# Kernel tuning notes

Hardware: AMD Instinct MI355X
Metric: run time of the kernel (lower is better)

## Reference

```python
import jax, jax.numpy as jnp
import numpy as np

B, V, C, NQ, H, PTS, FFN = 2, 6, 128, 1200, 8, 4, 256
SHAPES = [(112, 200), (56, 100), (28, 50), (14, 25)]
LVLS = len(SHAPES)
LTOT = sum(h * w for h, w in SHAPES)
STARTS = np.cumsum([0] + [h * w for h, w in SHAPES])[:-1].tolist()


def _ln(x, g, b):
    m = jnp.mean(x, -1, keepdims=True)
    v = jnp.var(x, -1, keepdims=True)
    return (x - m) * jax.lax.rsqrt(v + 1e-5) * g + b


def _mlp(x, w1, b1, w2, b2):
    return jax.nn.relu(x @ w1 + b1) @ w2 + b2


def setup_inputs():
    ks = iter(jax.random.split(jax.random.key(0), 64))
    def rn(*shape):
        return jax.random.normal(next(ks), shape, jnp.float32) * 0.02
    inp = {}
    inp["img_query_feat"] = jax.random.normal(next(ks), (B, C, NQ), jnp.float32)
    inp["normal_img_query_pos"] = jax.random.normal(next(ks), (B, NQ, 2), jnp.float32)
    for i, (h, w) in enumerate(SHAPES):
        inp["img_feat%d" % i] = jax.random.normal(next(ks), (B, V, C, h, w), jnp.float32)
    inp["normal_img_feats_pos_stack"] = jax.random.uniform(next(ks), (1, LTOT, 2), jnp.float32)
    inp["sp_w1"] = rn(2, C); inp["sp_b1"] = rn(C); inp["sp_w2"] = rn(C, C); inp["sp_b2"] = rn(C)
    inp["cp_w1"] = rn(2, C); inp["cp_b1"] = rn(C); inp["cp_w2"] = rn(C, C); inp["cp_b2"] = rn(C)
    inp["sa_wqkv"] = rn(C, 3 * C); inp["sa_bqkv"] = rn(3 * C); inp["sa_wo"] = rn(C, C); inp["sa_bo"] = rn(C)
    inp["ln1_g"] = jnp.ones((C,), jnp.float32); inp["ln1_b"] = jnp.zeros((C,), jnp.float32)
    inp["d_val_w"] = rn(C, C); inp["d_val_b"] = rn(C)
    inp["d_off_w"] = rn(C, H * LVLS * PTS * 2); inp["d_off_b"] = rn(H * LVLS * PTS * 2)
    inp["d_attn_w"] = rn(C, H * LVLS * PTS); inp["d_attn_b"] = rn(H * LVLS * PTS)
    inp["d_out_w"] = rn(C, C); inp["d_out_b"] = rn(C)
    inp["ln2_g"] = jnp.ones((C,), jnp.float32); inp["ln2_b"] = jnp.zeros((C,), jnp.float32)
    inp["ffn_w1"] = rn(C, FFN); inp["ffn_b1"] = rn(FFN); inp["ffn_w2"] = rn(FFN, C); inp["ffn_b2"] = rn(C)
    inp["ln3_g"] = jnp.ones((C,), jnp.float32); inp["ln3_b"] = jnp.zeros((C,), jnp.float32)
    inp["ph_w1"] = rn(C, C); inp["ph_b1"] = rn(C); inp["ph_w2"] = rn(C, 6); inp["ph_b2"] = rn(6)
    inp["img_query_view"] = jax.random.randint(next(ks), (B, NQ), 0, V)
    return inp


def _forward(img_query_view, img_query_feat, normal_img_query_pos, img_feat0, img_feat1, img_feat2, img_feat3, normal_img_feats_pos_stack, sp_w1, sp_b1, sp_w2, sp_b2, cp_w1, cp_b1, cp_w2, cp_b2, sa_wqkv, sa_bqkv, sa_wo, sa_bo, ln1_g, ln1_b, d_val_w, d_val_b, d_off_w, d_off_b, d_attn_w, d_attn_b, d_out_w, d_out_b, ln2_g, ln2_b, ffn_w1, ffn_b1, ffn_w2, ffn_b2, ln3_g, ln3_b, ph_w1, ph_b1, ph_w2, ph_b2):
    # flatten multi-scale feats: [B, V, C, LTOT]
    feats = jnp.concatenate([f.reshape(B, V, C, -1) for f in (img_feat0, img_feat1, img_feat2, img_feat3)], axis=3)
    ref = jax.nn.sigmoid(normal_img_query_pos)  # [B,NQ,2], shared across levels
    qpe = _mlp(normal_img_query_pos, sp_w1, sp_b1, sp_w2, sp_b2)  # [B,NQ,C] self posembed
    kpe = _mlp(normal_img_feats_pos_stack[0], cp_w1, cp_b1, cp_w2, cp_b2)  # [LTOT,C] cross posembed
    # value projection of (key + key_pos_embed), per view
    value = jnp.einsum('bvcl,cd->bvld', feats, d_val_w) + kpe @ d_val_w + d_val_b  # [B,V,LTOT,C]
    value_flat = value.reshape(B, V * LTOT, C)
    x = img_query_feat.transpose(0, 2, 1)  # [B,NQ,C]
    # ragged per-view grouping: queries interact only within their own view
    same_view = img_query_view[:, :, None] == img_query_view[:, None, :]
    counts = jax.vmap(lambda v: jnp.bincount(v, length=V))(img_query_view)  # [B,V]
    valid = jnp.take_along_axis(counts, img_query_view, axis=1) > 1  # views with <=1 query are skipped
    Ch = C // H
    # --- self attention (masked to same view) ---
    qkv = (x + qpe) @ sa_wqkv + sa_bqkv
    q, k, v = jnp.split(qkv, 3, axis=-1)
    q = q.reshape(B, NQ, H, Ch); k = k.reshape(B, NQ, H, Ch); v = v.reshape(B, NQ, H, Ch)
    logits = jnp.einsum('bnhd,bmhd->bhnm', q, k) / float(np.sqrt(Ch))
    logits = jnp.where(same_view[:, None], logits, -1e9)
    attn = jax.nn.softmax(logits, axis=-1)
    sa_out = jnp.einsum('bhnm,bmhd->bnhd', attn, v).reshape(B, NQ, C) @ sa_wo + sa_bo
    x = _ln(x + sa_out, ln1_g, ln1_b)
    # --- multi-scale deformable cross attention, view-routed per query ---
    qc = x + qpe
    off = (qc @ d_off_w + d_off_b).reshape(B, NQ, H, LVLS, PTS, 2)
    aw = jax.nn.softmax((qc @ d_attn_w + d_attn_b).reshape(B, NQ, H, LVLS * PTS), axis=-1).reshape(B, NQ, H, LVLS, PTS)
    normalizer = jnp.array([[w, h] for h, w in SHAPES], jnp.float32)  # (w,h) per level
    loc = ref[:, :, None, None, None, :] + off / normalizer[None, None, None, :, None, :]
    base = (img_query_view * LTOT)[:, :, None, None].astype(jnp.int32)  # route query to its view
    eyeH = jnp.eye(H, dtype=x.dtype)
    out = jnp.zeros((B, NQ, H, Ch), x.dtype)
    for l, (h, w) in enumerate(SHAPES):
        lx = loc[:, :, :, l, :, 0] * w - 0.5  # grid_sample align_corners=False convention
        ly = loc[:, :, :, l, :, 1] * h - 0.5  # [B,NQ,H,PTS]
        x0 = jnp.floor(lx); y0 = jnp.floor(ly)
        fx = lx - x0; fy = ly - y0
        x0i = x0.astype(jnp.int32); y0i = y0.astype(jnp.int32)
        samp = jnp.zeros((B, NQ, H, PTS, Ch), x.dtype)
        for dy in (0, 1):
            for dx in (0, 1):
                xi = x0i + dx; yi = y0i + dy
                wgt = (fx if dx else 1.0 - fx) * (fy if dy else 1.0 - fy)
                ok = (xi >= 0) & (xi < w) & (yi >= 0) & (yi < h)  # zero padding
                idx = base + STARTS[l] + jnp.clip(yi, 0, h - 1) * w + jnp.clip(xi, 0, w - 1)
                g = jnp.take_along_axis(value_flat, idx.reshape(B, -1)[:, :, None], axis=1)
                g = g.reshape(B, NQ, H, PTS, H, Ch)
                g = jnp.einsum('bnhpqc,hq->bnhpc', g, eyeH)  # head h uses its own channel slice
                samp = samp + jnp.where(ok[..., None], wgt[..., None], 0.0) * g
        out = out + jnp.einsum('bnhp,bnhpc->bnhc', aw[:, :, :, l], samp)
    ca_out = out.reshape(B, NQ, C) @ d_out_w + d_out_b
    x = _ln(x + ca_out, ln2_g, ln2_b)
    x = _ln(x + _mlp(x, ffn_w1, ffn_b1, ffn_w2, ffn_b2), ln3_g, ln3_b)
    x = jnp.where(valid[..., None], x, 0.0)  # skipped views stay zero (scatter-back semantics)
    # --- prediction head: center_offset [B,6,NQ] ---
    res = _mlp(x, ph_w1, ph_b1, ph_w2, ph_b2).transpose(0, 2, 1)
    center_raw = res[:, :2] + normal_img_query_pos.transpose(0, 2, 1)
    new_pos = jax.lax.stop_gradient(center_raw).transpose(0, 2, 1)  # supervision2d=True update
    center = jax.nn.sigmoid(center_raw)
    offs = jax.nn.sigmoid(res[:, 2:])
    bw = offs[:, 0] + offs[:, 2]
    bh = offs[:, 1] + offs[:, 3]
    cx = (2.0 * center[:, 0] - offs[:, 0] + offs[:, 2]) * 0.5
    cy = (2.0 * center[:, 1] - offs[:, 1] + offs[:, 3]) * 0.5
    bbox = jax.lax.stop_gradient(jnp.stack([cx, cy, bw, bh], axis=1))
    return (x.transpose(0, 2, 1), new_pos, center, offs, bbox)


def reference(img_query_feat, normal_img_query_pos, img_feat0, img_feat1, img_feat2, img_feat3, normal_img_feats_pos_stack, sp_w1, sp_b1, sp_w2, sp_b2, cp_w1, cp_b1, cp_w2, cp_b2, sa_wqkv, sa_bqkv, sa_wo, sa_bo, ln1_g, ln1_b, d_val_w, d_val_b, d_off_w, d_off_b, d_attn_w, d_attn_b, d_out_w, d_out_b, ln2_g, ln2_b, ffn_w1, ffn_b1, ffn_w2, ffn_b2, ln3_g, ln3_b, ph_w1, ph_b1, ph_w2, ph_b2, img_query_view):
    return _forward(img_query_view, img_query_feat, normal_img_query_pos, img_feat0, img_feat1, img_feat2, img_feat3, normal_img_feats_pos_stack, sp_w1, sp_b1, sp_w2, sp_b2, cp_w1, cp_b1, cp_w2, cp_b2, sa_wqkv, sa_bqkv, sa_wo, sa_bo, ln1_g, ln1_b, d_val_w, d_val_b, d_off_w, d_off_b, d_attn_w, d_attn_b, d_out_w, d_out_b, ln2_g, ln2_b, ffn_w1, ffn_b1, ffn_w2, ffn_b2, ln3_g, ln3_b, ph_w1, ph_b1, ph_w2, ph_b2)
```

## Files before the change

### kernel.cpp

```cpp
#include <hip/hip_runtime.h>
#include <hip/hip_bf16.h>
#include <math.h>

#define DEV __device__ __forceinline__

#define BB 2
#define VV 6
#define CC 128
#define NQ 1200
#define HH 8
#define PTSN 4
#define FFND 256
#define LVLSN 4
#define LTOT 29750
#define NROWS (BB*NQ)

__constant__ int c_W[4] = {200,100,50,25};
__constant__ int c_H[4] = {112,56,28,14};
__constant__ int c_S[4] = {0,22400,28000,29400};

DEV float bflo(unsigned u){ union{unsigned i; float f;}x; x.i = u<<16; return x.f; }
DEV float bfhi(unsigned u){ union{unsigned i; float f;}x; x.i = u&0xffff0000u; return x.f; }
DEV unsigned short f2bf(float f){ union{float f; unsigned i;}x; x.f=f; unsigned i=x.i;
  return (unsigned short)((i + 0x7fffu + ((i>>16)&1u))>>16); }
DEV unsigned addbf2(unsigned a, unsigned b){
  float lo = bflo(a)+bflo(b); float hi = bfhi(a)+bfhi(b);
  return (unsigned)f2bf(lo) | ((unsigned)f2bf(hi)<<16);
}
DEV float sigm(float z){ return 1.f/(1.f+__expf(-z)); }

typedef __attribute__((ext_vector_type(8))) short bf16x8;
typedef __attribute__((ext_vector_type(4))) float f32x4;

__global__ void k_misc(const int* __restrict__ view, int* __restrict__ order,
                       int* __restrict__ counts,
                       const float* __restrict__ vw, unsigned short* __restrict__ wt,
                       const float* __restrict__ cw2, unsigned short* __restrict__ cw2t,
                       const float* __restrict__ iqf, float* __restrict__ x,
                       const float* __restrict__ pos,
                       const float* __restrict__ w1, const float* __restrict__ b1,
                       const float* __restrict__ w2, const float* __restrict__ b2,
                       float* __restrict__ qpe){
  int bid = blockIdx.x;
  int t = threadIdx.x;
  if(bid < BB){
    if(t < 64){
      int b = bid; int lane = t;
      int base0=0,base1=0,base2=0,base3=0,base4=0,base5=0;
      for(int c0=0;c0<NQ;c0+=64){
        int n = c0 + lane;
        int v = (n<NQ) ? view[b*NQ+n] : -1;
        unsigned long long lower = (lane==63)? 0x7fffffffffffffffull : ((1ull<<lane)-1ull);
        #define BUCKET_STEP(VVV, BASE) { \
          unsigned long long mk = __ballot(v==VVV); \
          if(v==VVV){ int r = BASE + __popcll(mk & lower); order[(b*VV+VVV)*NQ + r] = n; } \
          BASE += __popcll(mk); }
        BUCKET_STEP(0, base0) BUCKET_STEP(1, base1) BUCKET_STEP(2, base2)
        BUCKET_STEP(3, base3) BUCKET_STEP(4, base4) BUCKET_STEP(5, base5)
        #undef BUCKET_STEP
      }
      if(lane==0){
        counts[b*VV+0]=base0; counts[b*VV+1]=base1; counts[b*VV+2]=base2;
        counts[b*VV+3]=base3; counts[b*VV+4]=base4; counts[b*VV+5]=base5;
      }
    }
  } else if(bid < BB+16){
    int d0 = (bid-BB)*8;
    __shared__ float s[128][9];
    #pragma unroll
    for(int p=0;p<4;p++){ int i = t + p*256; int c = i>>3, dd = i&7;
      s[c][dd] = vw[c*128 + d0 + dd]; }
    __syncthreads();
    #pragma unroll
    for(int p=0;p<4;p++){ int i = t + p*256; int dd = i>>7, c = i&127;
      wt[(size_t)(d0+dd)*128 + c] = f2bf(s[c][dd]); }
  } else if(bid < BB+32){
    int d0 = (bid-BB-16)*8;
    __shared__ float s[128][9];
    #pragma unroll
    for(int p=0;p<4;p++){ int i = t + p*256; int c = i>>3, dd = i&7;
      s[c][dd] = cw2[c*128 + d0 + dd]; }
    __syncthreads();
    #pragma unroll
    for(int p=0;p<4;p++){ int i = t + p*256; int dd = i>>7, c = i&127;
      cw2t[(size_t)(d0+dd)*128 + c] = f2bf(s[c][dd]); }
  } else if(bid < BB+32+76){
    __shared__ float tile[128][33];
    int idx = bid - (BB+32);
    int b = idx/38; int n0 = (idx%38)*32;
    for(int i=t;i<128*32;i+=256){ int c=i>>5, nn=i&31; int n=n0+nn;
      tile[c][nn] = (n<NQ)? iqf[((size_t)b*CC + c)*NQ + n] : 0.f; }
    __syncthreads();
    for(int i=t;i<32*128;i+=256){ int nn=i>>7, c=i&127;
      int n=n0+nn; if(n<NQ) x[((size_t)b*NQ+n)*128 + c] = tile[c][nn]; }
  } else {
    __shared__ float hid[4][128];
    int row0 = (bid - (BB+32+76))*4;
    int r = t>>7, d = t&127;
    #pragma unroll
    for(int rr=r; rr<4; rr+=2){
      int row = row0 + rr;
      float p0 = pos[row*2+0], p1 = pos[row*2+1];
      hid[rr][d] = fmaxf(p0*w1[d] + p1*w1[128+d] + b1[d], 0.f);
    }
    __syncthreads();
    #pragma unroll
    for(int rr=r; rr<4; rr+=2){
      float acc = b2[d];
      #pragma unroll 4
      for(int c=0;c<128;c++) acc += hid[rr][c]*w2[c*128 + d];
      qpe[(size_t)(row0+rr)*128+d] = acc;
    }
  }
}

__global__ void __launch_bounds__(256) k_kvpe2(
    const float* __restrict__ kpos,
    const float* __restrict__ cw1, const float* __restrict__ cb1,
    const unsigned short* __restrict__ cw2t, const float* __restrict__ cb2,
    const unsigned short* __restrict__ wt, const float* __restrict__ vb,
    unsigned short* __restrict__ kvpe){
  __shared__ unsigned short h_t[64][136];
  __shared__ unsigned short k_t[64][136];
  int t = threadIdx.x;
  int r0 = blockIdx.x*64;
  int lane = t&63, wave = t>>6;
  int fr = lane&15, kg = lane>>4;

  int p = t & 63;
  int d0 = p*2;
  float w1a0 = cw1[d0],     w1a1 = cw1[d0+1];
  float w1b0 = cw1[128+d0], w1b1 = cw1[128+d0+1];
  float b10 = cb1[d0], b11 = cb1[d0+1];
  #pragma unroll 4
  for(int k=0;k<16;k++){
    int r = wave + k*4;
    int row = r0 + r;
    float p0=0.f, p1=0.f;
    if(row < LTOT){ p0 = kpos[row*2]; p1 = kpos[row*2+1]; }
    float h0 = fmaxf(p0*w1a0 + p1*w1b0 + b10, 0.f);
    float h1 = fmaxf(p0*w1a1 + p1*w1b1 + b11, 0.f);
    *reinterpret_cast<unsigned*>(&h_t[r][d0]) = (unsigned)f2bf(h0) | ((unsigned)f2bf(h1)<<16);
  }
  __syncthreads();

  f32x4 acc[4][2];
  #pragma unroll
  for(int i=0;i<4;i++)
    #pragma unroll
    for(int j=0;j<2;j++) acc[i][j] = (f32x4)0.f;
  #pragma unroll
  for(int ck=0; ck<4; ck++){
    int c0 = ck*32;
    bf16x8 bfr[2], af[4];
    #pragma unroll
    for(int j=0;j<2;j++){ int d = wave*32 + j*16 + fr;
      bfr[j] = *reinterpret_cast<const bf16x8*>(cw2t + (size_t)d*128 + c0 + kg*8); }
    #pragma unroll
    for(int i=0;i<4;i++) af[i] = *reinterpret_cast<const bf16x8*>(&h_t[i*16 + fr][c0 + kg*8]);
    #pragma unroll
    for(int i=0;i<4;i++)
      #pragma unroll
      for(int j=0;j<2;j++)
        acc[i][j] = __builtin_amdgcn_mfma_f32_16x16x32_bf16(af[i], bfr[j], acc[i][j], 0, 0, 0);
  }
  #pragma unroll
  for(int i=0;i<4;i++){
    int rbase = i*16 + kg*4;
    #pragma unroll
    for(int j=0;j<2;j++){
      int d = wave*32 + j*16 + fr;
      float bv_ = cb2[d];
      #pragma unroll
      for(int r=0;r<4;r++) k_t[rbase + r][d] = f2bf(acc[i][j][r] + bv_);
    }
  }
  __syncthreads();

  #pragma unroll
  for(int i=0;i<4;i++)
    #pragma unroll
    for(int j=0;j<2;j++) acc[i][j] = (f32x4)0.f;
  #pragma unroll
  for(int ck=0; ck<4; ck++){
    int c0 = ck*32;
    bf16x8 bfr[2], af[4];
    #pragma unroll
    for(int j=0;j<2;j++){ int d = wave*32 + j*16 + fr;
      bfr[j] = *reinterpret_cast<const bf16x8*>(wt + (size_t)d*128 + c0 + kg*8); }
    #pragma unroll
    for(int i=0;i<4;i++) af[i] = *reinterpret_cast<const bf16x8*>(&k_t[i*16 + fr][c0 + kg*8]);
    #pragma unroll
    for(int i=0;i<4;i++)
      #pragma unroll
      for(int j=0;j<2;j++)
        acc[i][j] = __builtin_amdgcn_mfma_f32_16x16x32_bf16(af[i], bfr[j], acc[i][j], 0, 0, 0);
  }
  __syncthreads();
  unsigned short (*c_l)[136] = h_t;
  #pragma unroll
  for(int i=0;i<4;i++){
    int rbase = i*16 + kg*4;
    #pragma unroll
    for(int j=0;j<2;j++){
      int d = wave*32 + j*16 + fr;
      float bv_ = vb[d];
      #pragma unroll
      for(int r=0;r<4;r++) c_l[rbase + r][d] = f2bf(acc[i][j][r] + bv_);
    }
  }
  __syncthreads();
  #pragma unroll
  for(int p4=0;p4<4;p4++){
    int i = t + p4*256;
    int row = i>>4, seg = i&15;
    int glr = r0 + row;
    if(glr < LTOT){
      uint4 cu = *reinterpret_cast<const uint4*>(&c_l[row][seg*8]);
      *reinterpret_cast<uint4*>(kvpe + (size_t)glr*CC + seg*8) = cu;
    }
  }
}

#define QKVB 300
__global__ void __launch_bounds__(256) k_value_qkv(
    const float* __restrict__ f0, const float* __restrict__ f1,
    const float* __restrict__ f2, const float* __restrict__ f3,
    const unsigned short* __restrict__ kvpe, const unsigned short* __restrict__ wt,
    unsigned short* __restrict__ value,
    const float* __restrict__ x, const float* __restrict__ qpe,
    const float* __restrict__ sa_wqkv, const float* __restrict__ sa_bqkv,
    float* __restrict__ qkv){
  __shared__ unsigned short a_t[64][136];
  __shared__ float s_q[8][128];
  int t = threadIdx.x;
  int bid = blockIdx.x;
  if(bid < QKVB){
    int r0 = bid*8;
    for(int i=t;i<1024;i+=256){ int r=i>>7, c=i&127;
      size_t row = (size_t)(r0+r);
      s_q[r][c] = x[row*128+c] + qpe[row*128+c]; }
    __syncthreads();
    for(int d=t; d<384; d+=256){
      float acc[8];
      #pragma unroll
      for(int r=0;r<8;r++) acc[r]=sa_bqkv[d];
      #pragma unroll 4
      for(int c=0;c<128;c++){ float wv = sa_wqkv[c*384+d];
        #pragma unroll
        for(int r=0;r<8;r++) acc[r] += s_q[r][c]*wv; }
      #pragma unroll
      for(int r=0;r<8;r++) qkv[(size_t)(r0+r)*384+d]=acc[r];
    }
    return;
  }
  int bxy = bid - QKVB;
  int bv = bxy % 12;
  int bx = bxy / 12;
  int lvl, tile;
  if(bx < 350){ lvl=0; tile=bx; }
  else if(bx < 438){ lvl=1; tile=bx-350; }
  else if(bx < 460){ lvl=2; tile=bx-438; }
  else { lvl=3; tile=bx-460; }
  const int HW = (lvl==0)?22400:(lvl==1)?5600:(lvl==2)?1400:350;
  const int startL = (lvl==0)?0:(lvl==1)?22400:(lvl==2)?28000:29400;
  const float* feat = (lvl==0)?f0:(lvl==1)?f1:(lvl==2)?f2:f3;
  const float* fbase = feat + (size_t)bv*128*(size_t)HW;
  int l0 = tile*64;

  int lane = t&63, wave = t>>6;
  int fr = lane&15, kg = lane>>4;

  int l_u = t & 63, oct0 = t>>6;
  int gl = l0 + l_u; bool ok = (gl < HW);
  const float* fcol = fbase + (size_t)(oct0*8)*HW + (ok ? gl : 0);

  float v32[4][8];
  #pragma unroll
  for(int q=0;q<4;q++)
    #pragma unroll
    for(int j=0;j<8;j++)
      v32[q][j] = ok ? fcol[(size_t)(q*32+j)*HW] : 0.f;

  #pragma unroll
  for(int q=0;q<4;q++){
    uint4 u;
    u.x = (unsigned)f2bf(v32[q][0]) | ((unsigned)f2bf(v32[q][1])<<16);
    u.y = (unsigned)f2bf(v32[q][2]) | ((unsigned)f2bf(v32[q][3])<<16);
    u.z = (unsigned)f2bf(v32[q][4]) | ((unsigned)f2bf(v32[q][5])<<16);
    u.w = (unsigned)f2bf(v32[q][6]) | ((unsigned)f2bf(v32[q][7])<<16);
    *reinterpret_cast<uint4*>(&a_t[l_u][oct0*8 + q*32]) = u;
  }
  __syncthreads();

  f32x4 acc[4][2];
  #pragma unroll
  for(int i=0;i<4;i++)
    #pragma unroll
    for(int j=0;j<2;j++) acc[i][j] = (f32x4)0.f;

  #pragma unroll
  for(int ck=0; ck<4; ck++){
    int c0 = ck*32;
    bf16x8 bfr[2];
    #pragma unroll
    for(int j=0;j<2;j++){
      int d = wave*32 + j*16 + fr;
      bfr[j] = *reinterpret_cast<const bf16x8*>(wt + (size_t)d*128 + c0 + kg*8);
    }
    bf16x8 af[4];
    #pragma unroll
    for(int i=0;i<4;i++) af[i] = *reinterpret_cast<const bf16x8*>(&a_t[i*16 + fr][c0 + kg*8]);
    #pragma unroll
    for(int i=0;i<4;i++)
      #pragma unroll
      for(int j=0;j<2;j++)
        acc[i][j] = __builtin_amdgcn_mfma_f32_16x16x32_bf16(af[i], bfr[j], acc[i][j], 0, 0, 0);
  }

  __syncthreads();
  unsigned short (*c_l)[136] = a_t;
  #pragma unroll
  for(int i=0;i<4;i++){
    int rbase = i*16 + kg*4;
    #pragma unroll
    for(int j=0;j<2;j++){
      int d = wave*32 + j*16 + fr;
      #pragma unroll
      for(int r=0;r<4;r++) c_l[rbase + r][d] = f2bf(acc[i][j][r]);
    }
  }
  __syncthreads();
  #pragma unroll
  for(int p=0;p<4;p++){
    int i = t + p*256;
    int row = i>>4, seg = i&15;
    int glr = l0 + row;
    if(glr < HW){
      uint4 cu = *reinterpret_cast<const uint4*>(&c_l[row][seg*8]);
      const uint4 ku = *reinterpret_cast<const uint4*>(kvpe + (size_t)(startL+glr)*CC + seg*8);
      uint4 ou;
      ou.x = addbf2(cu.x, ku.x); ou.y = addbf2(cu.y, ku.y);
      ou.z = addbf2(cu.z, ku.z); ou.w = addbf2(cu.w, ku.w);
      *reinterpret_cast<uint4*>(value + ((size_t)bv*LTOT + startL + glr)*CC + seg*8) = ou;
    }
  }
}

#define QT2 64
#define KT2 128
__global__ void __launch_bounds__(256) k_attn_v(const float* __restrict__ qkv,
        const int* __restrict__ order, const int* __restrict__ counts,
        float* __restrict__ att){
  int qt = blockIdx.x;
  int vh = blockIdx.y; int v = vh>>3, h = vh&7;
  int b = blockIdx.z;
  int C = counts[b*VV+v];
  int q0 = qt*QT2;
  if(q0 >= C) return;
  const int* ord = order + (size_t)(b*VV+v)*NQ;
  int t = threadIdx.x;
  __shared__ float q_s[QT2][17];
  __shared__ int qn_s[QT2];
  __shared__ float k_s[KT2][16];
  __shared__ float v_s[KT2][16];
  __shared__ float red[4][QT2][18];
  for(int i=t;i<QT2;i+=256){ int qi=q0+i; qn_s[i] = (qi<C)? ord[qi] : -1; }
  __syncthreads();
  for(int i=t;i<QT2*16;i+=256){ int r=i>>4,c=i&15; int n=qn_s[r];
    q_s[r][c] = (n>=0)? qkv[((size_t)b*NQ+n)*384 + h*16 + c] : 0.f; }
  int qi = t&63, sub = t>>6;
  float m = -1e30f, s = 0.f, acc[16];
  #pragma unroll
  for(int c=0;c<16;c++) acc[c]=0.f;
  for(int k0=0; k0<C; k0+=KT2){
    int kn = C-k0; if(kn>KT2) kn=KT2;
    __syncthreads();
    for(int i=t;i<KT2*16;i+=256){ int r=i>>4,c=i&15;
      float kv=0.f, vv=0.f;
      if(r<kn){ int n=ord[k0+r]; size_t base=((size_t)b*NQ+n)*384 + h*16 + c;
        kv = qkv[base+128]; vv = qkv[base+256]; }
      k_s[r][c]=kv; v_s[r][c]=vv; }
    __syncthreads();
    for(int mm=sub; mm<kn; mm+=4){
      float l=0.f;
      #pragma unroll
      for(int c=0;c<16;c++) l += q_s[qi][c]*k_s[mm][c];
      l *= 0.25f;
      float newm = fmaxf(m,l);
      float e = __expf(l - newm);
      if(newm > m){
        float rr = __expf(m - newm);
        s *= rr;
        #pragma unroll
        for(int c=0;c<16;c++) acc[c]*=rr;
        m = newm;
      }
      s += e;
      #pragma unroll
      for(int c=0;c<16;c++) acc[c] += e*v_s[mm][c];
    }
  }
  red[sub][qi][0]=m; red[sub][qi][1]=s;
  #pragma unroll
  for(int c=0;c<16;c++) red[sub][qi][2+c]=acc[c];
  __syncthreads();
  if(sub==0){
    int n = qn_s[qi];
    if(n>=0){
      float M=-1e30f;
      #pragma unroll
      for(int j=0;j<4;j++) M=fmaxf(M,red[j][qi][0]);
      float S=0.f; float o[16];
      #pragma unroll
      for(int c=0;c<16;c++) o[c]=0.f;
      #pragma unroll
      for(int j=0;j<4;j++){ float e=__expf(red[j][qi][0]-M); S += e*red[j][qi][1];
        #pragma unroll
        for(int c=0;c<16;c++) o[c] += e*red[j][qi][2+c]; }
      float inv = 1.f/S;
      #pragma unroll
      for(int c=0;c<16;c++) att[((size_t)b*NQ+n)*128 + h*16 + c] = o[c]*inv;
    }
  }
}

__global__ void __launch_bounds__(384) k_q2(
    const float* __restrict__ att, const float* __restrict__ sa_wo, const float* __restrict__ sa_bo,
    float* __restrict__ x, const float* __restrict__ ln1_g, const float* __restrict__ ln1_b,
    const float* __restrict__ qpe,
    const float* __restrict__ dow, const float* __restrict__ dob,
    const float* __restrict__ daw, const float* __restrict__ dab,
    float* __restrict__ offb, float* __restrict__ awb){
  int r0 = blockIdx.x*8; int t = threadIdx.x;
  __shared__ float s_att[8][128];
  __shared__ float s_qc[8][128];
  __shared__ float s_m[8][2][2];
  __shared__ float s_aw[8][130];
  for(int i=t;i<1024;i+=384){ int r=i>>7, c=i&127; s_att[r][c]=att[(size_t)(r0+r)*128+c]; }
  __syncthreads();
  int lane = t&63, wid = (t>>6)&1;
  float v[8];
  if(t < 128){
    int d = t;
    float acc[8];
    #pragma unroll
    for(int r=0;r<8;r++) acc[r]=sa_bo[d];
    #pragma unroll 4
    for(int c=0;c<128;c++){ float wv = sa_wo[c*128+d];
      #pragma unroll
      for(int r=0;r<8;r++) acc[r] += s_att[r][c]*wv; }
    #pragma unroll
    for(int r=0;r<8;r++){
      v[r] = acc[r] + x[(size_t)(r0+r)*128 + d];
      float s1=v[r], s2=v[r]*v[r];
      for(int o=32;o>0;o>>=1){ s1 += __shfl_down(s1,o); s2 += __shfl_down(s2,o); }
      if(lane==0){ s_m[r][wid][0]=s1; s_m[r][wid][1]=s2; }
    }
  }
  __syncthreads();
  if(t < 128){
    int d = t;
    #pragma unroll
    for(int r=0;r<8;r++){
      float S1=s_m[r][0][0]+s_m[r][1][0], S2=s_m[r][0][1]+s_m[r][1][1];
      float mean=S1*(1.f/128.f), var=S2*(1.f/128.f)-mean*mean;
      float rs=rsqrtf(var+1e-5f);
      float o=(v[r]-mean)*rs*ln1_g[d]+ln1_b[d];
      x[(size_t)(r0+r)*128+d]=o;
      s_qc[r][d]=o+qpe[(size_t)(r0+r)*128+d];
    }
  }
  __syncthreads();
  if(t < 256){
    int d = t;
    float acc[8];
    #pragma unroll
    for(int r=0;r<8;r++) acc[r]=dob[d];
    #pragma unroll 4
    for(int c=0;c<128;c++){ float wv = dow[(size_t)c*256+d];
      #pragma unroll
      for(int r=0;r<8;r++) acc[r] += s_qc[r][c]*wv; }
    #pragma unroll
    for(int r=0;r<8;r++) offb[(size_t)(r0+r)*256+d]=acc[r];
  } else {
    int d = t - 256;
    float acc[8];
    #pragma unroll
    for(int r=0;r<8;r++) acc[r]=dab[d];
    #pragma unroll 4
    for(int c=0;c<128;c++){ float wv = daw[(size_t)c*128+d];
      #pragma unroll
      for(int r=0;r<8;r++) acc[r] += s_qc[r][c]*wv; }
    #pragma unroll
    for(int r=0;r<8;r++) s_aw[r][d]=acc[r];
  }
  __syncthreads();
  if(t < 64){
    int r = t>>3, h = t&7;
    float mx=-1e30f;
    #pragma unroll
    for(int i=0;i<16;i++) mx = fmaxf(mx, s_aw[r][h*16+i]);
    float e[16]; float sm=0.f;
    #pragma unroll
    for(int i=0;i<16;i++){ e[i]=__expf(s_aw[r][h*16+i]-mx); sm+=e[i]; }
    float inv = 1.f/sm;
    #pragma unroll
    for(int i=0;i<16;i++) awb[(size_t)(r0+r)*128 + h*16+i] = e[i]*inv;
  }
}

__global__ void k_sample(const float* __restrict__ qpos, const int* __restrict__ view,
                         const float* __restrict__ offb, const float* __restrict__ awb,
                         const unsigned short* __restrict__ value, float* __restrict__ ca){
  int n = blockIdx.x, b = blockIdx.y;
  size_t row = (size_t)b*NQ + n;
  int t = threadIdx.x;
  int h = t>>4, lp = t&15, lvl = lp>>2;
  float rx = sigm(qpos[row*2]), ry = sigm(qpos[row*2+1]);
  int vw = view[row];
  int w = c_W[lvl], hh = c_H[lvl];
  float ox = offb[row*256 + t*2], oy = offb[row*256 + t*2+1];
  float a = awb[row*128 + t];
  float lx = rx*(float)w + ox - 0.5f;
  float ly = ry*(float)hh + oy - 0.5f;
  float x0f = floorf(lx), y0f = floorf(ly);
  float fx = lx - x0f, fy = ly - y0f;
  int x0 = (int)x0f, y0 = (int)y0f;
  float samp[16];
  #pragma unroll
  for(int c=0;c<16;c++) samp[c]=0.f;
  size_t brow = ((size_t)(b*VV + vw))*LTOT + c_S[lvl];
  #pragma unroll
  for(int dy=0;dy<2;dy++){
    #pragma unroll
    for(int dx=0;dx<2;dx++){
      int xi=x0+dx, yi=y0+dy;
      if(xi<0||xi>=w||yi<0||yi>=hh) continue;
      float wt = (dx?fx:(1.f-fx))*(dy?fy:(1.f-fy));
      const uint4* vp = reinterpret_cast<const uint4*>(value + (brow + (size_t)yi*w + xi)*CC + h*16);
      uint4 u0 = vp[0], u1 = vp[1];
      samp[0] += wt*bflo(u0.x); samp[1] += wt*bfhi(u0.x);
      samp[2] += wt*bflo(u0.y); samp[3] += wt*bfhi(u0.y);
      samp[4] += wt*bflo(u0.z); samp[5] += wt*bfhi(u0.z);
      samp[6] += wt*bflo(u0.w); samp[7] += wt*bfhi(u0.w);
      samp[8] += wt*bflo(u1.x); samp[9] += wt*bfhi(u1.x);
      samp[10]+= wt*bflo(u1.y); samp[11]+= wt*bfhi(u1.y);
      samp[12]+= wt*bflo(u1.z); samp[13]+= wt*bfhi(u1.z);
      samp[14]+= wt*bflo(u1.w); samp[15]+= wt*bfhi(u1.w);
    }
  }
  __shared__ float sred[128][17];
  #pragma unroll
  for(int c=0;c<16;c++) sred[t][c] = a*samp[c];
  __syncthreads();
  int h2=t>>4, c2=t&15;
  float sum=0.f;
  #pragma unroll
  for(int j=0;j<16;j++) sum += sred[h2*16+j][c2];
  ca[row*128 + t] = sum;
}

__global__ void __launch_bounds__(128) k_tail(
    const float* __restrict__ ca, const float* __restrict__ dOw, const float* __restrict__ dOb,
    const float* __restrict__ xres,
    const float* __restrict__ ln2_g, const float* __restrict__ ln2_b,
    const float* __restrict__ fw1, const float* __restrict__ fb1,
    const float* __restrict__ fw2, const float* __restrict__ fb2,
    const float* __restrict__ ln3_g, const float* __restrict__ ln3_b,
    const float* __restrict__ pw1, const float* __restrict__ pb1,
    const float* __restrict__ pw2, const float* __restrict__ pb2,
    const int* __restrict__ counts, const int* __restrict__ view,
    const float* __restrict__ pos, float* __restrict__ dout){
  int r0 = blockIdx.x*4; int d = threadIdx.x;
  __shared__ float s_a[4][256];
  __shared__ float s_x[4][128];
  __shared__ float s_m[4][2][2];
  __shared__ float s_res[4][6];
  int lane = d&63, wid = d>>6;

  #pragma unroll
  for(int r=0;r<4;r++) s_a[r][d] = ca[(size_t)(r0+r)*128 + d];
  __syncthreads();

  float acc[4];
  #pragma unroll
  for(int r=0;r<4;r++) acc[r]=dOb[d];
  #pragma unroll 4
  for(int c=0;c<128;c++){ float wv = dOw[c*128+d];
    #pragma unroll
    for(int r=0;r<4;r++) acc[r] += s_a[r][c]*wv; }
  float v[4];
  #pragma unroll
  for(int r=0;r<4;r++){
    v[r] = acc[r] + xres[(size_t)(r0+r)*128 + d];
    float s1=v[r], s2=v[r]*v[r];
    for(int o=32;o>0;o>>=1){ s1 += __shfl_down(s1,o); s2 += __shfl_down(s2,o); }
    if(lane==0){ s_m[r][wid][0]=s1; s_m[r][wid][1]=s2; }
  }
  __syncthreads();
  #pragma unroll
  for(int r=0;r<4;r++){
    float S1=s_m[r][0][0]+s_m[r][1][0], S2=s_m[r][0][1]+s_m[r][1][1];
    float mean=S1*(1.f/128.f), var=S2*(1.f/128.f)-mean*mean;
    float rs=rsqrtf(var+1e-5f);
    s_x[r][d]=(v[r]-mean)*rs*ln2_g[d]+ln2_b[d];
  }
  __syncthreads();

  float a2a[4], a2b[4];
  #pragma unroll
  for(int r=0;r<4;r++){ a2a[r]=fb1[d]; a2b[r]=fb1[d+128]; }
  #pragma unroll 4
  for(int c=0;c<128;c++){ float w0 = fw1[c*256+d], w1_ = fw1[c*256+d+128];
    #pragma unroll
    for(int r=0;r<4;r++){ float xv = s_x[r][c]; a2a[r] += xv*w0; a2b[r] += xv*w1_; } }
  __syncthreads();
  #pragma unroll
  for(int r=0;r<4;r++){ s_a[r][d]=fmaxf(a2a[r],0.f); s_a[r][d+128]=fmaxf(a2b[r],0.f); }
  __syncthreads();

  float a3[4];
  #pragma unroll
  for(int r=0;r<4;r++) a3[r]=fb2[d];
  #pragma unroll 4
  for(int c=0;c<256;c++){ float wv = fw2[c*128+d];
    #pragma unroll
    for(int r=0;r<4;r++) a3[r] += s_a[r][c]*wv; }
  #pragma unroll
  for(int r=0;r<4;r++){
    v[r] = a3[r] + s_x[r][d];
    float s1=v[r], s2=v[r]*v[r];
    for(int o=32;o>0;o>>=1){ s1 += __shfl_down(s1,o); s2 += __shfl_down(s2,o); }
    if(lane==0){ s_m[r][wid][0]=s1; s_m[r][wid][1]=s2; }
  }
  __syncthreads();
  #pragma unroll
  for(int r=0;r<4;r++){
    float S1=s_m[r][0][0]+s_m[r][1][0], S2=s_m[r][0][1]+s_m[r][1][1];
    float mean=S1*(1.f/128.f), var=S2*(1.f/128.f)-mean*mean;
    float rs=rsqrtf(var+1e-5f);
    float o=(v[r]-mean)*rs*ln3_g[d]+ln3_b[d];
    int row=r0+r; int b=row/NQ, n=row%NQ;
    bool val = counts[b*VV + view[row]] > 1;
    float oz = val ? o : 0.f;
    s_x[r][d]=oz;
    dout[((size_t)b*CC + d)*NQ + n]=oz;
  }
  __syncthreads();

  float a4[4];
  #pragma unroll
  for(int r=0;r<4;r++) a4[r]=pb1[d];
  #pragma unroll 4
  for(int c=0;c<128;c++){ float wv = pw1[c*128+d];
    #pragma unroll
    for(int r=0;r<4;r++) a4[r] += s_x[r][c]*wv; }
  #pragma unroll
  for(int r=0;r<4;r++) s_a[r][d]=fmaxf(a4[r],0.f);
  __syncthreads();

  if(d < 24){
    int r = d/6, o = d%6;
    float a5 = pb2[o];
    #pragma unroll 4
    for(int c=0;c<128;c++) a5 += s_a[r][c]*pw2[c*6+o];
    s_res[r][o] = a5;
  }
  __syncthreads();
  if(d < 4){
    int r = d; int row = r0+r; int b=row/NQ, n=row%NQ;
    const int O1 = BB*CC*NQ;
    const int O2 = O1 + BB*NQ*2;
    const int O3 = O2 + BB*2*NQ;
    const int O4 = O3 + BB*4*NQ;
    float p0=pos[row*2], p1=pos[row*2+1];
    float cr0 = s_res[r][0]+p0, cr1 = s_res[r][1]+p1;
    dout[O1 + row*2]   = cr0;
    dout[O1 + row*2+1] = cr1;
    float cen0 = sigm(cr0), cen1 = sigm(cr1);
    dout[O2 + (b*2+0)*NQ + n] = cen0;
    dout[O2 + (b*2+1)*NQ + n] = cen1;
    float f0=sigm(s_res[r][2]), f1=sigm(s_res[r][3]), f2=sigm(s_res[r][4]), f3=sigm(s_res[r][5]);
    dout[O3 + (b*4+0)*NQ + n] = f0;
    dout[O3 + (b*4+1)*NQ + n] = f1;
    dout[O3 + (b*4+2)*NQ + n] = f2;
    dout[O3 + (b*4+3)*NQ + n] = f3;
    float bw=f0+f2, bh=f1+f3;
    float cx=(2.f*cen0 - f0 + f2)*0.5f;
    float cy=(2.f*cen1 - f1 + f3)*0.5f;
    dout[O4 + (b*4+0)*NQ + n] = cx;
    dout[O4 + (b*4+1)*NQ + n] = cy;
    dout[O4 + (b*4+2)*NQ + n] = bw;
    dout[O4 + (b*4+3)*NQ + n] = bh;
  }
}

extern "C" void kernel_launch(void* const* d_in, const int* in_sizes, int n_in,
                              void* d_out, int out_size, void* d_ws, size_t ws_size,
                              hipStream_t stream){
  (void)in_sizes; (void)n_in; (void)out_size; (void)ws_size;
  const float* in_iqf  = (const float*)d_in[0];
  const float* in_qpos = (const float*)d_in[1];
  const float* in_feat[4] = {(const float*)d_in[2],(const float*)d_in[3],(const float*)d_in[4],(const float*)d_in[5]};
  const float* in_kpos = (const float*)d_in[6];
  const float* sp_w1=(const float*)d_in[7], *sp_b1=(const float*)d_in[8], *sp_w2=(const float*)d_in[9], *sp_b2=(const float*)d_in[10];
  const float* cp_w1=(const float*)d_in[11], *cp_b1=(const float*)d_in[12], *cp_w2=(const float*)d_in[13], *cp_b2=(const float*)d_in[14];
  const float* sa_wqkv=(const float*)d_in[15], *sa_bqkv=(const float*)d_in[16], *sa_wo=(const float*)d_in[17], *sa_bo=(const float*)d_in[18];
  const float* ln1_g=(const float*)d_in[19], *ln1_b=(const float*)d_in[20];
  const float* dvw=(const float*)d_in[21], *dvb=(const float*)d_in[22];
  const float* dow=(const float*)d_in[23], *dob=(const float*)d_in[24];
  const float* daw=(const float*)d_in[25], *dab=(const float*)d_in[26];
  const float* dOw=(const float*)d_in[27], *dOb=(const float*)d_in[28];
  const float* ln2_g=(const float*)d_in[29], *ln2_b=(const float*)d_in[30];
  const float* fw1=(const float*)d_in[31], *fb1=(const float*)d_in[32], *fw2=(const float*)d_in[33], *fb2=(const float*)d_in[34];
  const float* ln3_g=(const float*)d_in[35], *ln3_b=(const float*)d_in[36];
  const float* pw1=(const float*)d_in[37], *pb1=(const float*)d_in[38], *pw2=(const float*)d_in[39], *pb2=(const float*)d_in[40];
  const int* in_view = (const int*)d_in[41];
  float* out = (float*)d_out;

  char* ws = (char*)d_ws;
  unsigned short* value = (unsigned short*)ws;
  unsigned short* kvpe  = (unsigned short*)(ws + 91392000);
  float* f = (float*)(ws + 91392000 + 7616000);
  float* qpe  = f;
  float* x    = f + 307200;
  float* qkv  = f + 614400;
  float* att  = f + 1536000;
  float* offb = f + 2150400;
  float* awb  = f + 2764800;
  float* ca   = f + 3072000;
  int* counts = (int*)(f + 4300800);
  int* order  = (int*)(f + 4300816);
  unsigned short* wtb   = (unsigned short*)(f + 4315216);
  unsigned short* cw2tb = (unsigned short*)(f + 4323408);

  k_misc<<<dim3(BB+32+76+600),dim3(256),0,stream>>>(in_view,order,counts,dvw,wtb,
      cp_w2,cw2tb,in_iqf,x,in_qpos,sp_w1,sp_b1,sp_w2,sp_b2,qpe);
  k_kvpe2<<<dim3((LTOT+63)/64),dim3(256),0,stream>>>(in_kpos,cp_w1,cp_b1,cw2tb,cp_b2,wtb,dvb,kvpe);
  k_value_qkv<<<dim3(QKVB + 466*12),dim3(256),0,stream>>>(in_feat[0],in_feat[1],in_feat[2],in_feat[3],
      kvpe,wtb,value,x,qpe,sa_wqkv,sa_bqkv,qkv);
  k_attn_v<<<dim3((NQ+QT2-1)/QT2, VV*HH, BB),dim3(256),0,stream>>>(qkv,order,counts,att);
  k_q2<<<dim3(NROWS/8),dim3(384),0,stream>>>(att,sa_wo,sa_bo,x,ln1_g,ln1_b,qpe,
      dow,dob,daw,dab,offb,awb);
  k_sample<<<dim3(NQ,BB),dim3(128),0,stream>>>(in_qpos,in_view,offb,awb,value,ca);
  k_tail<<<dim3(NROWS/4),dim3(128),0,stream>>>(ca,dOw,dOb,x,ln2_g,ln2_b,
      fw1,fb1,fw2,fb2,ln3_g,ln3_b,pw1,pb1,pw2,pb2,counts,in_view,in_qpos,out);
}
```

Baseline: 226.0 us.

## Fuse QKV projection into attention blocks and deformable sampling into tail kernel

Result: slower. 390.3 us (+72.7%).

```diff
diff --git a/kernel.cpp b/kernel.cpp
--- a/kernel.cpp
+++ b/kernel.cpp
@@ -222,39 +222,112 @@
   }
 }
 
-#define QKVB 300
-__global__ void __launch_bounds__(256) k_value_qkv(
+#define NATT (19*48*2)
+__global__ void __launch_bounds__(256) k_value_attn(
     const float* __restrict__ f0, const float* __restrict__ f1,
     const float* __restrict__ f2, const float* __restrict__ f3,
     const unsigned short* __restrict__ kvpe, const unsigned short* __restrict__ wt,
     unsigned short* __restrict__ value,
     const float* __restrict__ x, const float* __restrict__ qpe,
     const float* __restrict__ sa_wqkv, const float* __restrict__ sa_bqkv,
-    float* __restrict__ qkv){
-  __shared__ unsigned short a_t[64][136];
-  __shared__ float s_q[8][128];
+    const int* __restrict__ order, const int* __restrict__ counts,
+    float* __restrict__ att){
+  __shared__ __align__(16) char smem[45568];
   int t = threadIdx.x;
   int bid = blockIdx.x;
-  if(bid < QKVB){
-    int r0 = bid*8;
-    for(int i=t;i<1024;i+=256){ int r=i>>7, c=i&127;
-      size_t row = (size_t)(r0+r);
-      s_q[r][c] = x[row*128+c] + qpe[row*128+c]; }
-    __syncthreads();
-    for(int d=t; d<384; d+=256){
-      float acc[8];
-      #pragma unroll
-      for(int r=0;r<8;r++) acc[r]=sa_bqkv[d];
+  if(bid < NATT){
+    int qt = bid % 19;
+    int vh = (bid/19) % 48;
+    int b  = bid/(19*48);
+    int v = vh>>3, h = vh&7;
+    int C = counts[b*VV+v];
+    int q0 = qt*64;
+    if(q0 >= C) return;
+    const int* ord = order + (size_t)(b*VV+v)*NQ;
+    float (*xq_s)[128] = (float(*)[128])smem;
+    float (*red)[64][18] = (float(*)[64][18])smem;
+    float (*k_s)[16] = (float(*)[16])(smem + 32768);
+    float (*v_s)[16] = (float(*)[16])(smem + 36864);
+    float (*q_s)[17] = (float(*)[17])(smem + 40960);
+    int* qn_s = (int*)(smem + 45312);
+    int hh16 = h*16;
+    for(int i=t;i<64;i+=256){ int qi=q0+i; qn_s[i] = (qi<C)? ord[qi] : -1; }
+    __syncthreads();
+    for(int i=t;i<8192;i+=256){ int r=i>>7, c=i&127; int n=qn_s[r];
+      float vv=0.f;
+      if(n>=0){ size_t rw=((size_t)b*NQ+n)*128+c; vv = x[rw]+qpe[rw]; }
+      xq_s[r][c]=vv; }
+    __syncthreads();
+    for(int i=t;i<1024;i+=256){ int r=i>>4, c16=i&15;
+      float a = sa_bqkv[hh16+c16];
       #pragma unroll 4
-      for(int c=0;c<128;c++){ float wv = sa_wqkv[c*384+d];
+      for(int c=0;c<128;c++) a += xq_s[r][c]*sa_wqkv[c*384 + hh16 + c16];
+      q_s[r][c16]=a; }
+    int qi = t&63, sub = t>>6;
+    float m = -1e30f, s = 0.f, acc[16];
+    #pragma unroll
+    for(int c=0;c<16;c++) acc[c]=0.f;
+    for(int k0=0; k0<C; k0+=64){
+      int kn = C-k0; if(kn>64) kn=64;
+      __syncthreads();
+      for(int i=t;i<8192;i+=256){ int r=i>>7, c=i&127;
+        float vv=0.f;
+        if(r<kn){ int n=ord[k0+r]; size_t rw=((size_t)b*NQ+n)*128+c; vv = x[rw]+qpe[rw]; }
+        xq_s[r][c]=vv; }
+      __syncthreads();
+      for(int i=t;i<2048;i+=256){ int r=i>>5, j=i&31; int kv=j>>4, c16=j&15;
+        int od = 128 + kv*128 + hh16 + c16;
+        float a = sa_bqkv[od];
+        #pragma unroll 4
+        for(int c=0;c<128;c++) a += xq_s[r][c]*sa_wqkv[c*384 + od];
+        if(kv==0) k_s[r][c16]=a; else v_s[r][c16]=a; }
+      __syncthreads();
+      for(int mm=sub; mm<kn; mm+=4){
+        float l=0.f;
         #pragma unroll
-        for(int r=0;r<8;r++) acc[r] += s_q[r][c]*wv; }
-      #pragma unroll
-      for(int r=0;r<8;r++) qkv[(size_t)(r0+r)*384+d]=acc[r];
+        for(int c=0;c<16;c++) l += q_s[qi][c]*k_s[mm][c];
+        l *= 0.25f;
+        float newm = fmaxf(m,l);
+        float e = __expf(l - newm);
+        if(newm > m){
+          float rr = __expf(m - newm);
+          s *= rr;
+          #pragma unroll
+          for(int c=0;c<16;c++) acc[c]*=rr;
+          m = newm;
+        }
+        s += e;
+        #pragma unroll
+        for(int c=0;c<16;c++) acc[c] += e*v_s[mm][c];
+      }
+    }
+    __syncthreads();
+    red[sub][qi][0]=m; red[sub][qi][1]=s;
+    #pragma unroll
+    for(int c=0;c<16;c++) red[sub][qi][2+c]=acc[c];
+    __syncthreads();
+    if(sub==0){
+      int n = qn_s[qi];
+      if(n>=0){
+        float M=-1e30f;
+        #pragma unroll
+        for(int j=0;j<4;j++) M=fmaxf(M,red[j][qi][0]);
+        float S=0.f; float o[16];
+        #pragma unroll
+        for(int c=0;c<16;c++) o[c]=0.f;
+        #pragma unroll
+        for(int j=0;j<4;j++){ float e=__expf(red[j][qi][0]-M); S += e*red[j][qi][1];
+          #pragma unroll
+          for(int c=0;c<16;c++) o[c] += e*red[j][qi][2+c]; }
+        float inv = 1.f/S;
+        #pragma unroll
+        for(int c=0;c<16;c++) att[((size_t)b*NQ+n)*128 + hh16 + c] = o[c]*inv;
+      }
     }
     return;
   }
-  int bxy = bid - QKVB;
+  unsigned short (*a_t)[136] = (unsigned short(*)[136])smem;
+  int bxy = bid - NATT;
   int bv = bxy % 12;
   int bx = bxy / 12;
   int lvl, tile;
@@ -343,84 +416,6 @@
       ou.x = addbf2(cu.x, ku.x); ou.y = addbf2(cu.y, ku.y);
       ou.z = addbf2(cu.z, ku.z); ou.w = addbf2(cu.w, ku.w);
       *reinterpret_cast<uint4*>(value + ((size_t)bv*LTOT + startL + glr)*CC + seg*8) = ou;
-    }
-  }
-}
-
-#define QT2 64
-#define KT2 128
-__global__ void __launch_bounds__(256) k_attn_v(const float* __restrict__ qkv,
-        const int* __restrict__ order, const int* __restrict__ counts,
-        float* __restrict__ att){
-  int qt = blockIdx.x;
-  int vh = blockIdx.y; int v = vh>>3, h = vh&7;
-  int b = blockIdx.z;
-  int C = counts[b*VV+v];
-  int q0 = qt*QT2;
-  if(q0 >= C) return;
-  const int* ord = order + (size_t)(b*VV+v)*NQ;
-  int t = threadIdx.x;
-  __shared__ float q_s[QT2][17];
-  __shared__ int qn_s[QT2];
-  __shared__ float k_s[KT2][16];
-  __shared__ float v_s[KT2][16];
-  __shared__ float red[4][QT2][18];
-  for(int i=t;i<QT2;i+=256){ int qi=q0+i; qn_s[i] = (qi<C)? ord[qi] : -1; }
-  __syncthreads();
-  for(int i=t;i<QT2*16;i+=256){ int r=i>>4,c=i&15; int n=qn_s[r];
-    q_s[r][c] = (n>=0)? qkv[((size_t)b*NQ+n)*384 + h*16 + c] : 0.f; }
-  int qi = t&63, sub = t>>6;
-  float m = -1e30f, s = 0.f, acc[16];
-  #pragma unroll
-  for(int c=0;c<16;c++) acc[c]=0.f;
-  for(int k0=0; k0<C; k0+=KT2){
-    int kn = C-k0; if(kn>KT2) kn=KT2;
-    __syncthreads();
-    for(int i=t;i<KT2*16;i+=256){ int r=i>>4,c=i&15;
-      float kv=0.f, vv=0.f;
-      if(r<kn){ int n=ord[k0+r]; size_t base=((size_t)b*NQ+n)*384 + h*16 + c;
-        kv = qkv[base+128]; vv = qkv[base+256]; }
-      k_s[r][c]=kv; v_s[r][c]=vv; }
-    __syncthreads();
-    for(int mm=sub; mm<kn; mm+=4){
-      float l=0.f;
-      #pragma unroll
-      for(int c=0;c<16;c++) l += q_s[qi][c]*k_s[mm][c];
-      l *= 0.25f;
-      float newm = fmaxf(m,l);
-      float e = __expf(l - newm);
-      if(newm > m){
-        float rr = __expf(m - newm);
-        s *= rr;
-        #pragma unroll
-        for(int c=0;c<16;c++) acc[c]*=rr;
-        m = newm;
-      }
-      s += e;
-      #pragma unroll
-      for(int c=0;c<16;c++) acc[c] += e*v_s[mm][c];
-    }
-  }
-  red[sub][qi][0]=m; red[sub][qi][1]=s;
-  #pragma unroll
-  for(int c=0;c<16;c++) red[sub][qi][2+c]=acc[c];
-  __syncthreads();
-  if(sub==0){
-    int n = qn_s[qi];
-    if(n>=0){
-      float M=-1e30f;
-      #pragma unroll
-      for(int j=0;j<4;j++) M=fmaxf(M,red[j][qi][0]);
-      float S=0.f; float o[16];
-      #pragma unroll
-      for(int c=0;c<16;c++) o[c]=0.f;
-      #pragma unroll
-      for(int j=0;j<4;j++){ float e=__expf(red[j][qi][0]-M); S += e*red[j][qi][1];
-        #pragma unroll
-        for(int c=0;c<16;c++) o[c] += e*red[j][qi][2+c]; }
-      float inv = 1.f/S;
-      #pragma unroll
-      for(int c=0;c<16;c++) att[((size_t)b*NQ+n)*128 + h*16 + c] = o[c]*inv;
     }
   }
 }
@@ -510,59 +505,11 @@
   }
 }
 
-__global__ void k_sample(const float* __restrict__ qpos, const int* __restrict__ view,
-                         const float* __restrict__ offb, const float* __restrict__ awb,
-                         const unsigned short* __restrict__ value, float* __restrict__ ca){
-  int n = blockIdx.x, b = blockIdx.y;
-  size_t row = (size_t)b*NQ + n;
-  int t = threadIdx.x;
-  int h = t>>4, lp = t&15, lvl = lp>>2;
-  float rx = sigm(qpos[row*2]), ry = sigm(qpos[row*2+1]);
-  int vw = view[row];
-  int w = c_W[lvl], hh = c_H[lvl];
-  float ox = offb[row*256 + t*2], oy = offb[row*256 + t*2+1];
-  float a = awb[row*128 + t];
-  float lx = rx*(float)w + ox - 0.5f;
-  float ly = ry*(float)hh + oy - 0.5f;
-  float x0f = floorf(lx), y0f = floorf(ly);
-  float fx = lx - x0f, fy = ly - y0f;
-  int x0 = (int)x0f, y0 = (int)y0f;
-  float samp[16];
-  #pragma unroll
-  for(int c=0;c<16;c++) samp[c]=0.f;
-  size_t brow = ((size_t)(b*VV + vw))*LTOT + c_S[lvl];
-  #pragma unroll
-  for(int dy=0;dy<2;dy++){
-    #pragma unroll
-    for(int dx=0;dx<2;dx++){
-      int xi=x0+dx, yi=y0+dy;
-      if(xi<0||xi>=w||yi<0||yi>=hh) continue;
-      float wt = (dx?fx:(1.f-fx))*(dy?fy:(1.f-fy));
-      const uint4* vp = reinterpret_cast<const uint4*>(value + (brow + (size_t)yi*w + xi)*CC + h*16);
-      uint4 u0 = vp[0], u1 = vp[1];
-      samp[0] += wt*bflo(u0.x); samp[1] += wt*bfhi(u0.x);
-      samp[2] += wt*bflo(u0.y); samp[3] += wt*bfhi(u0.y);
-      samp[4] += wt*bflo(u0.z); samp[5] += wt*bfhi(u0.z);
-      samp[6] += wt*bflo(u0.w); samp[7] += wt*bfhi(u0.w);
-      samp[8] += wt*bflo(u1.x); samp[9] += wt*bfhi(u1.x);
-      samp[10]+= wt*bflo(u1.y); samp[11]+= wt*bfhi(u1.y);
-      samp[12]+= wt*bflo(u1.z); samp[13]+= wt*bfhi(u1.z);
-      samp[14]+= wt*bflo(u1.w); samp[15]+= wt*bfhi(u1.w);
-    }
-  }
-  __shared__ float sred[128][17];
-  #pragma unroll
-  for(int c=0;c<16;c++) sred[t][c] = a*samp[c];
-  __syncthreads();
-  int h2=t>>4, c2=t&15;
-  float sum=0.f;
-  #pragma unroll
-  for(int j=0;j<16;j++) sum += sred[h2*16+j][c2];
-  ca[row*128 + t] = sum;
-}
-
-__global__ void __launch_bounds__(128) k_tail(
-    const float* __restrict__ ca, const float* __restrict__ dOw, const float* __restrict__ dOb,
+__global__ void __launch_bounds__(128) k_tail2(
+    const float* __restrict__ qpos, const int* __restrict__ view,
+    const float* __restrict__ offb, const float* __restrict__ awb,
+    const unsigned short* __restrict__ value,
+    const float* __restrict__ dOw, const float* __restrict__ dOb,
     const float* __restrict__ xres,
     const float* __restrict__ ln2_g, const float* __restrict__ ln2_b,
     const float* __restrict__ fw1, const float* __restrict__ fb1,
@@ -570,19 +517,72 @@
     const float* __restrict__ ln3_g, const float* __restrict__ ln3_b,
     const float* __restrict__ pw1, const float* __restrict__ pb1,
     const float* __restrict__ pw2, const float* __restrict__ pb2,
-    const int* __restrict__ counts, const int* __restrict__ view,
-    const float* __restrict__ pos, float* __restrict__ dout){
+    const int* __restrict__ counts, float* __restrict__ dout){
   int r0 = blockIdx.x*4; int d = threadIdx.x;
   __shared__ float s_a[4][256];
   __shared__ float s_x[4][128];
   __shared__ float s_m[4][2][2];
   __shared__ float s_res[4][6];
+  __shared__ float sred[128][17];
+  __shared__ float s_ca[4][128];
   int lane = d&63, wid = d>>6;
 
-  #pragma unroll
-  for(int r=0;r<4;r++) s_a[r][d] = ca[(size_t)(r0+r)*128 + d];
-  __syncthreads();
-
+  int h = d>>4, lp = d&15, lvl = lp>>2;
+  int w = c_W[lvl], hh = c_H[lvl];
+  float samp[4][16]; float aw4[4];
+  int vw4[4];
+  #pragma unroll
+  for(int r=0;r<4;r++){
+    size_t row = (size_t)(r0+r);
+    int b = (r0+r)/NQ;
+    float rx = sigm(qpos[row*2]), ry = sigm(qpos[row*2+1]);
+    int vw = view[row]; vw4[r]=vw;
+    float ox = offb[row*256 + d*2], oy = offb[row*256 + d*2+1];
+    aw4[r] = awb[row*128 + d];
+    float lx = rx*(float)w + ox - 0.5f;
+    float ly = ry*(float)hh + oy - 0.5f;
+    float x0f = floorf(lx), y0f = floorf(ly);
+    float fx = lx - x0f, fy = ly - y0f;
+    int x0 = (int)x0f, y0 = (int)y0f;
+    #pragma unroll
+    for(int c=0;c<16;c++) samp[r][c]=0.f;
+    size_t brow = ((size_t)(b*VV + vw))*LTOT + c_S[lvl];
+    #pragma unroll
+    for(int dy=0;dy<2;dy++){
+      #pragma unroll
+      for(int dx=0;dx<2;dx++){
+        int xi=x0+dx, yi=y0+dy;
+        if(xi<0||xi>=w||yi<0||yi>=hh) continue;
+        float wt = (dx?fx:(1.f-fx))*(dy?fy:(1.f-fy));
+        const uint4* vp = reinterpret_cast<const uint4*>(value + (brow + (size_t)yi*w + xi)*CC + h*16);
+        uint4 u0 = vp[0], u1 = vp[1];
+        samp[r][0] += wt*bflo(u0.x); samp[r][1] += wt*bfhi(u0.x);
+        samp[r][2] += wt*bflo(u0.y); samp[r][3] += wt*bfhi(u0.y);
+        samp[r][4] += wt*bflo(u0.z); samp[r][5] += wt*bfhi(u0.z);
+        samp[r][6] += wt*bflo(u0.w); samp[r][7] += wt*bfhi(u0.w);
+        samp[r][8] += wt*bflo(u1.x); samp[r][9] += wt*bfhi(u1.x);
+        samp[r][10]+= wt*bflo(u1.y); samp[r][11]+= wt*bfhi(u1.y);
+        samp[r][12]+= wt*bflo(u1.z); samp[r][13]+= wt*bfhi(u1.z);
+        samp[r][14]+= wt*bflo(u1.w); samp[r][15]+= wt*bfhi(u1.w);
+      }
+    }
+  }
+  #pragma unroll
+  for(int r=0;r<4;r++){
+    #pragma unroll
+    for(int c=0;c<16;c++) sred[d][c] = aw4[r]*samp[r][c];
+    __syncthreads();
+    int h2=d>>4, c2=d&15;
+    float sum=0.f;
+    #pragma unroll
+    for(int j=0;j<16;j++) sum += sred[h2*16+j][c2];
+    s_ca[r][d] = sum;
+    __syncthreads();
+  }
+
+  #pragma unroll
+  for(int r=0;r<4;r++) s_a[r][d] = s_ca[r][d];
+  __syncthreads();
   float acc[4];
   #pragma unroll
   for(int r=0;r<4;r++) acc[r]=dOb[d];
@@ -642,7 +642,7 @@
     float rs=rsqrtf(var+1e-5f);
     float o=(v[r]-mean)*rs*ln3_g[d]+ln3_b[d];
     int row=r0+r; int b=row/NQ, n=row%NQ;
-    bool val = counts[b*VV + view[row]] > 1;
+    bool val = counts[b*VV + vw4[r]] > 1;
     float oz = val ? o : 0.f;
     s_x[r][d]=oz;
     dout[((size_t)b*CC + d)*NQ + n]=oz;
@@ -674,7 +674,7 @@
     const int O2 = O1 + BB*NQ*2;
     const int O3 = O2 + BB*2*NQ;
     const int O4 = O3 + BB*4*NQ;
-    float p0=pos[row*2], p1=pos[row*2+1];
+    float p0=qpos[row*2], p1=qpos[row*2+1];
     float cr0 = s_res[r][0]+p0, cr1 = s_res[r][1]+p1;
     dout[O1 + row*2]   = cr0;
     dout[O1 + row*2+1] = cr1;
@@ -725,11 +725,9 @@
   float* f = (float*)(ws + 91392000 + 7616000);
   float* qpe  = f;
   float* x    = f + 307200;
-  float* qkv  = f + 614400;
   float* att  = f + 1536000;
   float* offb = f + 2150400;
   float* awb  = f + 2764800;
-  float* ca   = f + 3072000;
   int* counts = (int*)(f + 4300800);
   int* order  = (int*)(f + 4300816);
   unsigned short* wtb   = (unsigned short*)(f + 4315216);
@@ -738,12 +736,10 @@
   k_misc<<<dim3(BB+32+76+600),dim3(256),0,stream>>>(in_view,order,counts,dvw,wtb,
       cp_w2,cw2tb,in_iqf,x,in_qpos,sp_w1,sp_b1,sp_w2,sp_b2,qpe);
   k_kvpe2<<<dim3((LTOT+63)/64),dim3(256),0,stream>>>(in_kpos,cp_w1,cp_b1,cw2tb,cp_b2,wtb,dvb,kvpe);
-  k_value_qkv<<<dim3(QKVB + 466*12),dim3(256),0,stream>>>(in_feat[0],in_feat[1],in_feat[2],in_feat[3],
-      kvpe,wtb,value,x,qpe,sa_wqkv,sa_bqkv,qkv);
-  k_attn_v<<<dim3((NQ+QT2-1)/QT2, VV*HH, BB),dim3(256),0,stream>>>(qkv,order,counts,att);
+  k_value_attn<<<dim3(NATT + 466*12),dim3(256),0,stream>>>(in_feat[0],in_feat[1],in_feat[2],in_feat[3],
+      kvpe,wtb,value,x,qpe,sa_wqkv,sa_bqkv,order,counts,att);
   k_q2<<<dim3(NROWS/8),dim3(384),0,stream>>>(att,sa_wo,sa_bo,x,ln1_g,ln1_b,qpe,
       dow,dob,daw,dab,offb,awb);
-  k_sample<<<dim3(NQ,BB),dim3(128),0,stream>>>(in_qpos,in_view,offb,awb,value,ca);
-  k_tail<<<dim3(NROWS/4),dim3(128),0,stream>>>(ca,dOw,dOb,x,ln2_g,ln2_b,
-      fw1,fb1,fw2,fb2,ln3_g,ln3_b,pw1,pb1,pw2,pb2,counts,in_view,in_qpos,out);
+  k_tail2<<<dim3(NROWS/4),dim3(128),0,stream>>>(in_qpos,in_view,offb,awb,value,
+      dOw,dOb,x,ln2_g,ln2_b,fw1,fb1,fw2,fb2,ln3_g,ln3_b,pw1,pb1,pw2,pb2,counts,out);
 }
```
